# Kernel optimization log

Measured on AMD Instinct MI355X. Metric: run time of the kernel, lower is better.

The kernel has to match this reference:

```python
import jax, jax.numpy as jnp
import numpy as np

N_HEADS = 4
D_HEAD = 32  # out_features // n_heads = 128 // 4
NEG_SLOPE = 0.2


def setup_inputs() -> dict:
    key = jax.random.key(0)
    k_x, k_adj, k_w, k_a = jax.random.split(key, 4)
    B, N, F_in, F_out = 4, 2048, 128, 128
    x = jax.random.normal(k_x, (B, N, F_in), dtype=jnp.float32)
    adj = jax.random.randint(k_adj, (B, N, N), 0, 2, dtype=jnp.int32)
    # Linear weight stored as [in, out] (torch stores [out, in]; math identical: x @ W)
    w_scale = np.sqrt(2.0 / (F_in + F_out))  # xavier-ish
    W = jax.random.normal(k_w, (F_in, F_out), dtype=jnp.float32) * w_scale
    a = jax.random.normal(k_a, (N_HEADS, 2 * D_HEAD), dtype=jnp.float32) * np.sqrt(2.0 / (2 * D_HEAD))
    return {"x": x, "adj": adj, "W": W, "a": a}


def reference(x, adj, W, a):
    B, N, _ = x.shape
    # project and split heads: [B, H, N, D]
    h = jnp.einsum('bnf,fo->bno', x, W).reshape(B, N, N_HEADS, D_HEAD).transpose(0, 2, 1, 3)
    # additive attention logits
    e_src = jnp.einsum('bhnd,hd->bhn', h, a[:, :D_HEAD])  # [B,H,N]
    e_dst = jnp.einsum('bhnd,hd->bhn', h, a[:, D_HEAD:])  # [B,H,N]
    e = e_src[:, :, :, None] + e_dst[:, :, None, :]       # [B,H,N,N]
    e = jnp.where(e > 0, e, NEG_SLOPE * e)                # leaky_relu(0.2)
    mask = (adj[:, None, :, :] == 0)                      # [B,1,N,N] -> broadcast over heads
    e = jnp.where(mask, -jnp.inf, e)
    alpha = jax.nn.softmax(e, axis=-1)                    # dropout omitted (eval mode)
    out = jnp.einsum('bhnm,bhmd->bhnd', alpha, h)         # weighted aggregation
    out = out.transpose(0, 2, 1, 3).reshape(B, N, N_HEADS * D_HEAD)
    return jax.nn.elu(out)
```

## Files before the change

kernel.cpp:

```cpp
#include <hip/hip_runtime.h>
#include <hip/hip_bf16.h>

#define BB 4
#define NN 2048
#define FIN 128
#define NH 4
#define DH 32
#define NS 0.2f

typedef unsigned int u32;
typedef unsigned short u16;
typedef unsigned long long u64;
typedef __attribute__((ext_vector_type(8))) short short8;
typedef __attribute__((ext_vector_type(4))) float f32x4;

#define OFF_ES 0
#define OFF_ED 32768
#define OFF_P  65536
#define OFF_Q  98304
#define OFF_M  131072
#define OFF_HT 131088
#define OFF_BITS 655376

__device__ __forceinline__ u16 f2bf_rne(float f) {
  unsigned u = __float_as_uint(f);
  return (u16)((u + 0x7fffu + ((u >> 16) & 1u)) >> 16);
}

__global__ __launch_bounds__(256) void k_pack(const int* __restrict__ adj,
                                              u32* __restrict__ bits) {
  const int row = (blockIdx.x << 2) | (threadIdx.x >> 6);
  const int lane = threadIdx.x & 63;
  const int* src = adj + (size_t)row * NN;
  u32* dst = bits + (size_t)row * 64;
#pragma unroll 8
  for (int it = 0; it < 32; ++it) {
    const int v = src[it * 64 + lane];
    const u64 m = __ballot(v != 0);
    if (lane == 0) *(u64*)(dst + it * 2) = m;
  }
}

__global__ __launch_bounds__(256) void k_proj(
    const float* __restrict__ x, const float* __restrict__ W,
    const float* __restrict__ a, u16* __restrict__ hT,
    float* __restrict__ e_src, float* __restrict__ e_dst) {
  __shared__ float Ws[FIN * 128];
  const int tid = threadIdx.x;
  const int f = tid & 127, g = tid >> 7;
  const float4* Wg4 = (const float4*)W;
  float4* Ws4 = (float4*)Ws;
#pragma unroll
  for (int t = 0; t < 16; ++t) Ws4[t * 256 + tid] = Wg4[t * 256 + tid];
  __syncthreads();

  const int rb = blockIdx.x * 16 + g * 8;
  const int head = f >> 5, d = f & 31;
  const int b = rb >> 11, n0 = rb & (NN - 1);
  const int bh = b * NH + head;
  const float a_s = a[head * (2 * DH) + d];
  const float a_d = a[head * (2 * DH) + DH + d];

  float acc[8];
#pragma unroll
  for (int r = 0; r < 8; ++r) acc[r] = 0.f;

  const float* xb = x + (size_t)rb * FIN;
  for (int k = 0; k < FIN; ++k) {
    const float wv = Ws[k * 128 + f];
#pragma unroll
    for (int r = 0; r < 8; ++r) acc[r] = fmaf(wv, xb[r * FIN + k], acc[r]);
  }

  u16 hs[8];
#pragma unroll
  for (int r = 0; r < 8; ++r) hs[r] = f2bf_rne(acc[r]);
  u16* dst = hT + ((size_t)bh * DH + d) * NN + n0;
  *(int4*)dst = *(int4*)&hs[0];

#pragma unroll
  for (int r = 0; r < 8; ++r) {
    float s1 = acc[r] * a_s;
    float s2 = acc[r] * a_d;
#pragma unroll
    for (int off = 16; off >= 1; off >>= 1) {
      s1 += __shfl_xor(s1, off);
      s2 += __shfl_xor(s2, off);
    }
    if (d == 0) {
      e_src[(size_t)bh * NN + n0 + r] = s1;
      e_dst[(size_t)bh * NN + n0 + r] = s2;
    }
  }
}

__global__ __launch_bounds__(64) void k_prep(
    const float* __restrict__ e_dst, float* __restrict__ P,
    float* __restrict__ Q, float* __restrict__ M) {
  const int bh = blockIdx.x >> 3, seg = blockIdx.x & 7;
  const int lane = threadIdx.x;
  const float* ed = e_dst + (size_t)bh * NN;
  float m = -1e30f;
#pragma unroll
  for (int t = 0; t < 32; ++t) m = fmaxf(m, ed[t * 64 + lane]);
#pragma unroll
  for (int off = 32; off >= 1; off >>= 1) m = fmaxf(m, __shfl_xor(m, off));
  if (seg == 0 && lane == 0) M[bh] = m;
#pragma unroll
  for (int t = 0; t < 4; ++t) {
    const int j = seg * 256 + t * 64 + lane;
    const float e = ed[j];
    P[(size_t)bh * NN + j] = __expf(e);
    Q[(size_t)bh * NN + j] = __expf(NS * e);
  }
}

__global__ __launch_bounds__(256) void k_attn(
    const u16* __restrict__ hT, const float* __restrict__ e_src,
    const float* __restrict__ Pv, const float* __restrict__ Qv,
    const float* __restrict__ Mv, const u32* __restrict__ bits,
    float* __restrict__ out) {
  __shared__ float part[4][32][33];
  __shared__ float sp[4][2][16];

  const int bid = blockIdx.x;
  const int bh = bid >> 6;
  const int it = bid & 63;
  const int b = bh >> 2, head = bh & 3;

  const int w = threadIdx.x >> 6;
  const int lane = threadIdx.x & 63;
  const int lg = lane >> 4, lm = lane & 15;

  const int i0 = it * 32 + lm;
  const int i1 = i0 + 16;
  const float m = Mv[bh];
  const float es0 = e_src[(size_t)bh * NN + i0];
  const float es1 = e_src[(size_t)bh * NN + i1];
  const float mr0 = es0 + m, mr1 = es1 + m;
  const float mi0 = fmaxf(mr0, NS * mr0), mi1 = fmaxf(mr1, NS * mr1);
  const float A0 = __expf(es0 - mi0), B0 = __expf(NS * es0 - mi0);
  const float A1 = __expf(es1 - mi1), B1 = __expf(NS * es1 - mi1);
  const float T0 = __expf(-es0), T1 = __expf(-es1);

  const float* Pb = Pv + (size_t)bh * NN;
  const float* Qb = Qv + (size_t)bh * NN;
  const u16* hb0 = hT + ((size_t)bh * DH + lm) * NN;
  const u16* hb1 = hT + ((size_t)bh * DH + 16 + lm) * NN;
  const u32* br0 = bits + ((size_t)b * NN + i0) * 64 + w * 16;
  const u32* br1 = bits + ((size_t)b * NN + i1) * 64 + w * 16;
  const int shamt = lg * 8;

  f32x4 acc00 = {0,0,0,0}, acc01 = {0,0,0,0};
  f32x4 acc10 = {0,0,0,0}, acc11 = {0,0,0,0};
  float S0 = 0.f, S1 = 0.f;

  const int jbase = w * 512 + lg * 8;
  for (int jo = 0; jo < 4; ++jo) {
    const int4 bq0 = *(const int4*)(br0 + jo * 4);
    const int4 bq1 = *(const int4*)(br1 + jo * 4);
    const int wa0[4] = {bq0.x, bq0.y, bq0.z, bq0.w};
    const int wa1[4] = {bq1.x, bq1.y, bq1.z, bq1.w};
#pragma unroll
    for (int ju = 0; ju < 4; ++ju) {
      const int jj = jbase + jo * 128 + ju * 32;
      const float4 p0 = *(const float4*)(Pb + jj);
      const float4 p1 = *(const float4*)(Pb + jj + 4);
      const float4 q0 = *(const float4*)(Qb + jj);
      const float4 q1 = *(const float4*)(Qb + jj + 4);
      const short8 hv0 = *(const short8*)(hb0 + jj);
      const short8 hv1 = *(const short8*)(hb1 + jj);
      const u32 wsh0 = ((u32)wa0[ju]) >> shamt;
      const u32 wsh1 = ((u32)wa1[ju]) >> shamt;
      const float pp[8] = {p0.x, p0.y, p0.z, p0.w, p1.x, p1.y, p1.z, p1.w};
      const float qq[8] = {q0.x, q0.y, q0.z, q0.w, q1.x, q1.y, q1.z, q1.w};
      short8 af0, af1;
#pragma unroll
      for (int e = 0; e < 8; ++e) {
        const int m0 = (int)(wsh0 << (31 - e)) >> 31;
        const int m1 = (int)(wsh1 << (31 - e)) >> 31;
        const bool c0 = pp[e] > T0;
        float w0 = (c0 ? A0 : B0) * (c0 ? pp[e] : qq[e]);
        w0 = __int_as_float(__float_as_int(w0) & m0);
        S0 += w0;
        af0[e] = (short)__builtin_bit_cast(unsigned short, __float2bfloat16(w0));
        const bool c1 = pp[e] > T1;
        float w1 = (c1 ? A1 : B1) * (c1 ? pp[e] : qq[e]);
        w1 = __int_as_float(__float_as_int(w1) & m1);
        S1 += w1;
        af1[e] = (short)__builtin_bit_cast(unsigned short, __float2bfloat16(w1));
      }
      acc00 = __builtin_amdgcn_mfma_f32_16x16x32_bf16(af0, hv0, acc00, 0, 0, 0);
      acc01 = __builtin_amdgcn_mfma_f32_16x16x32_bf16(af0, hv1, acc01, 0, 0, 0);
      acc10 = __builtin_amdgcn_mfma_f32_16x16x32_bf16(af1, hv0, acc10, 0, 0, 0);
      acc11 = __builtin_amdgcn_mfma_f32_16x16x32_bf16(af1, hv1, acc11, 0, 0, 0);
    }
  }

  S0 += __shfl_xor(S0, 16); S0 += __shfl_xor(S0, 32);
  S1 += __shfl_xor(S1, 16); S1 += __shfl_xor(S1, 32);

#pragma unroll
  for (int r = 0; r < 4; ++r) {
    const int rl = lg * 4 + r;
    part[w][rl][lm] = acc00[r];
    part[w][rl][16 + lm] = acc01[r];
    part[w][16 + rl][lm] = acc10[r];
    part[w][16 + rl][16 + lm] = acc11[r];
  }
  if (lg == 0) { sp[w][0][lm] = S0; sp[w][1][lm] = S1; }
  __syncthreads();

  const int tid = threadIdx.x;
#pragma unroll
  for (int t = 0; t < 4; ++t) {
    const int idx = t * 256 + tid;
    const int row = idx >> 5, d = idx & 31;
    const float v = part[0][row][d] + part[1][row][d] +
                    part[2][row][d] + part[3][row][d];
    const float s = sp[0][row >> 4][row & 15] + sp[1][row >> 4][row & 15] +
                    sp[2][row >> 4][row & 15] + sp[3][row >> 4][row & 15];
    const float o = v / s;
    const int n = it * 32 + row;
    out[((size_t)b * NN + n) * 128 + head * 32 + d] =
        o > 0.f ? o : (__expf(o) - 1.f);
  }
}

extern "C" void kernel_launch(void* const* d_in, const int* in_sizes, int n_in,
                              void* d_out, int out_size, void* d_ws, size_t ws_size,
                              hipStream_t stream) {
  const float* x = (const float*)d_in[0];
  const int* adj = (const int*)d_in[1];
  const float* W = (const float*)d_in[2];
  const float* a = (const float*)d_in[3];
  float* out = (float*)d_out;
  float* ws = (float*)d_ws;

  float* e_src = ws + OFF_ES;
  float* e_dst = ws + OFF_ED;
  float* Pv = ws + OFF_P;
  float* Qv = ws + OFF_Q;
  float* Mv = ws + OFF_M;
  u16* hT = (u16*)(ws + OFF_HT);
  u32* bits = (u32*)(ws + OFF_BITS);

  k_pack<<<(BB * NN) / 4, 256, 0, stream>>>(adj, bits);
  k_proj<<<(BB * NN) / 16, 256, 0, stream>>>(x, W, a, hT, e_src, e_dst);
  k_prep<<<BB * NH * 8, 64, 0, stream>>>(e_dst, Pv, Qv, Mv);
  k_attn<<<BB * NH * 64, 256, 0, stream>>>(hT, e_src, Pv, Qv, Mv, bits, out);
}
```

Measured before the change: 69.05 us.

## Merge pack and projection kernels; simplify attention weight computation with fmax

Fuses the adjacency bit-packing and projection kernels into a single launch, interleaving one projection block with four packing blocks, so one launch is dropped and the two workloads overlap. In the attention loop, the branchy leaky-relu select becomes fmax(A*P, B*Q), which removes the per-row threshold exp. The loop is also flattened to 16 chunks with per-chunk bitmask loads, and the MFMA issue is wrapped in s_setprio. Every packing block still reserves the 64KB LDS array, which may limit occupancy for those blocks.

```diff
diff --git a/kernel.cpp b/kernel.cpp
--- a/kernel.cpp
+++ b/kernel.cpp
@@ -27,26 +27,31 @@
   return (u16)((u + 0x7fffu + ((u >> 16) & 1u)) >> 16);
 }
 
-__global__ __launch_bounds__(256) void k_pack(const int* __restrict__ adj,
-                                              u32* __restrict__ bits) {
-  const int row = (blockIdx.x << 2) | (threadIdx.x >> 6);
-  const int lane = threadIdx.x & 63;
-  const int* src = adj + (size_t)row * NN;
-  u32* dst = bits + (size_t)row * 64;
-#pragma unroll 8
-  for (int it = 0; it < 32; ++it) {
-    const int v = src[it * 64 + lane];
-    const u64 m = __ballot(v != 0);
-    if (lane == 0) *(u64*)(dst + it * 2) = m;
-  }
-}
-
-__global__ __launch_bounds__(256) void k_proj(
+__global__ __launch_bounds__(256) void k_pp(
+    const int* __restrict__ adj, u32* __restrict__ bits,
     const float* __restrict__ x, const float* __restrict__ W,
     const float* __restrict__ a, u16* __restrict__ hT,
     float* __restrict__ e_src, float* __restrict__ e_dst) {
   __shared__ float Ws[FIN * 128];
+  const int bid = blockIdx.x;
   const int tid = threadIdx.x;
+
+  if (bid % 5 != 0) {
+    const int pid = bid - bid / 5 - 1;
+    const int row = (pid << 2) | (tid >> 6);
+    const int lane = tid & 63;
+    const int* src = adj + (size_t)row * NN;
+    u32* dst = bits + (size_t)row * 64;
+#pragma unroll 8
+    for (int it = 0; it < 32; ++it) {
+      const int v = src[it * 64 + lane];
+      const u64 m = __ballot(v != 0);
+      if (lane == 0) *(u64*)(dst + it * 2) = m;
+    }
+    return;
+  }
+
+  const int pid = bid / 5;
   const int f = tid & 127, g = tid >> 7;
   const float4* Wg4 = (const float4*)W;
   float4* Ws4 = (float4*)Ws;
@@ -54,7 +59,7 @@
   for (int t = 0; t < 16; ++t) Ws4[t * 256 + tid] = Wg4[t * 256 + tid];
   __syncthreads();
 
-  const int rb = blockIdx.x * 16 + g * 8;
+  const int rb = pid * 16 + g * 8;
   const int head = f >> 5, d = f & 31;
   const int b = rb >> 11, n0 = rb & (NN - 1);
   const int bh = b * NH + head;
@@ -141,7 +146,6 @@
   const float mi0 = fmaxf(mr0, NS * mr0), mi1 = fmaxf(mr1, NS * mr1);
   const float A0 = __expf(es0 - mi0), B0 = __expf(NS * es0 - mi0);
   const float A1 = __expf(es1 - mi1), B1 = __expf(NS * es1 - mi1);
-  const float T0 = __expf(-es0), T1 = __expf(-es1);
 
   const float* Pb = Pv + (size_t)bh * NN;
   const float* Qb = Qv + (size_t)bh * NN;
@@ -156,45 +160,39 @@
   float S0 = 0.f, S1 = 0.f;
 
   const int jbase = w * 512 + lg * 8;
-  for (int jo = 0; jo < 4; ++jo) {
-    const int4 bq0 = *(const int4*)(br0 + jo * 4);
-    const int4 bq1 = *(const int4*)(br1 + jo * 4);
-    const int wa0[4] = {bq0.x, bq0.y, bq0.z, bq0.w};
-    const int wa1[4] = {bq1.x, bq1.y, bq1.z, bq1.w};
-#pragma unroll
-    for (int ju = 0; ju < 4; ++ju) {
-      const int jj = jbase + jo * 128 + ju * 32;
-      const float4 p0 = *(const float4*)(Pb + jj);
-      const float4 p1 = *(const float4*)(Pb + jj + 4);
-      const float4 q0 = *(const float4*)(Qb + jj);
-      const float4 q1 = *(const float4*)(Qb + jj + 4);
-      const short8 hv0 = *(const short8*)(hb0 + jj);
-      const short8 hv1 = *(const short8*)(hb1 + jj);
-      const u32 wsh0 = ((u32)wa0[ju]) >> shamt;
-      const u32 wsh1 = ((u32)wa1[ju]) >> shamt;
-      const float pp[8] = {p0.x, p0.y, p0.z, p0.w, p1.x, p1.y, p1.z, p1.w};
-      const float qq[8] = {q0.x, q0.y, q0.z, q0.w, q1.x, q1.y, q1.z, q1.w};
-      short8 af0, af1;
-#pragma unroll
-      for (int e = 0; e < 8; ++e) {
-        const int m0 = (int)(wsh0 << (31 - e)) >> 31;
-        const int m1 = (int)(wsh1 << (31 - e)) >> 31;
-        const bool c0 = pp[e] > T0;
-        float w0 = (c0 ? A0 : B0) * (c0 ? pp[e] : qq[e]);
-        w0 = __int_as_float(__float_as_int(w0) & m0);
-        S0 += w0;
-        af0[e] = (short)__builtin_bit_cast(unsigned short, __float2bfloat16(w0));
-        const bool c1 = pp[e] > T1;
-        float w1 = (c1 ? A1 : B1) * (c1 ? pp[e] : qq[e]);
-        w1 = __int_as_float(__float_as_int(w1) & m1);
-        S1 += w1;
-        af1[e] = (short)__builtin_bit_cast(unsigned short, __float2bfloat16(w1));
-      }
-      acc00 = __builtin_amdgcn_mfma_f32_16x16x32_bf16(af0, hv0, acc00, 0, 0, 0);
-      acc01 = __builtin_amdgcn_mfma_f32_16x16x32_bf16(af0, hv1, acc01, 0, 0, 0);
-      acc10 = __builtin_amdgcn_mfma_f32_16x16x32_bf16(af1, hv0, acc10, 0, 0, 0);
-      acc11 = __builtin_amdgcn_mfma_f32_16x16x32_bf16(af1, hv1, acc11, 0, 0, 0);
-    }
+#pragma unroll 2
+  for (int ch = 0; ch < 16; ++ch) {
+    const int jj = jbase + ch * 32;
+    const u32 wsh0 = br0[ch] >> shamt;
+    const u32 wsh1 = br1[ch] >> shamt;
+    const float4 p0 = *(const float4*)(Pb + jj);
+    const float4 p1 = *(const float4*)(Pb + jj + 4);
+    const float4 q0 = *(const float4*)(Qb + jj);
+    const float4 q1 = *(const float4*)(Qb + jj + 4);
+    const short8 hv0 = *(const short8*)(hb0 + jj);
+    const short8 hv1 = *(const short8*)(hb1 + jj);
+    const float pp[8] = {p0.x, p0.y, p0.z, p0.w, p1.x, p1.y, p1.z, p1.w};
+    const float qq[8] = {q0.x, q0.y, q0.z, q0.w, q1.x, q1.y, q1.z, q1.w};
+    short8 af0, af1;
+#pragma unroll
+    for (int e = 0; e < 8; ++e) {
+      const int m0 = (int)(wsh0 << (31 - e)) >> 31;
+      const int m1 = (int)(wsh1 << (31 - e)) >> 31;
+      float w0 = fmaxf(A0 * pp[e], B0 * qq[e]);
+      w0 = __int_as_float(__float_as_int(w0) & m0);
+      S0 += w0;
+      af0[e] = (short)__builtin_bit_cast(unsigned short, __float2bfloat16(w0));
+      float w1 = fmaxf(A1 * pp[e], B1 * qq[e]);
+      w1 = __int_as_float(__float_as_int(w1) & m1);
+      S1 += w1;
+      af1[e] = (short)__builtin_bit_cast(unsigned short, __float2bfloat16(w1));
+    }
+    __builtin_amdgcn_s_setprio(1);
+    acc00 = __builtin_amdgcn_mfma_f32_16x16x32_bf16(af0, hv0, acc00, 0, 0, 0);
+    acc01 = __builtin_amdgcn_mfma_f32_16x16x32_bf16(af0, hv1, acc01, 0, 0, 0);
+    acc10 = __builtin_amdgcn_mfma_f32_16x16x32_bf16(af1, hv0, acc10, 0, 0, 0);
+    acc11 = __builtin_amdgcn_mfma_f32_16x16x32_bf16(af1, hv1, acc11, 0, 0, 0);
+    __builtin_amdgcn_s_setprio(0);
   }
 
   S0 += __shfl_xor(S0, 16); S0 += __shfl_xor(S0, 32);
@@ -245,8 +243,7 @@
   u16* hT = (u16*)(ws + OFF_HT);
   u32* bits = (u32*)(ws + OFF_BITS);
 
-  k_pack<<<(BB * NN) / 4, 256, 0, stream>>>(adj, bits);
-  k_proj<<<(BB * NN) / 16, 256, 0, stream>>>(x, W, a, hT, e_src, e_dst);
+  k_pp<<<2560, 256, 0, stream>>>(adj, bits, x, W, a, hT, e_src, e_dst);
   k_prep<<<BB * NH * 8, 64, 0, stream>>>(e_dst, Pv, Qv, Mv);
   k_attn<<<BB * NH * 64, 256, 0, stream>>>(hT, e_src, Pv, Qv, Mv, bits, out);
 }
```

After: 106.6 us. 1.54x slower.

## Halve rows per attention block, use fmax for leaky-relu weights, raise MFMA priority

Applied to the files above, without the earlier changes.

Each attention block now handles 16 query rows instead of 32, which doubles the grid to 2048 blocks and halves per-thread register and accumulator state. The compare-and-select form of the leaky-relu exponent weight is replaced by fmaxf(A*P, B*Q), which relies on exp being monotonic and drops the T threshold exp. s_setprio brackets the MFMA calls so they are favoured when waves compete. In exchange, each block reloads the P, Q and hT data for only half as many rows, so global/L2 traffic per output row doubles.

```diff
diff --git a/kernel.cpp b/kernel.cpp
--- a/kernel.cpp
+++ b/kernel.cpp
@@ -120,47 +120,39 @@
     const float* __restrict__ Pv, const float* __restrict__ Qv,
     const float* __restrict__ Mv, const u32* __restrict__ bits,
     float* __restrict__ out) {
-  __shared__ float part[4][32][33];
-  __shared__ float sp[4][2][16];
+  __shared__ float part[4][16][33];
+  __shared__ float sp[4][16];
 
   const int bid = blockIdx.x;
-  const int bh = bid >> 6;
-  const int it = bid & 63;
+  const int bh = bid >> 7;
+  const int it = bid & 127;
   const int b = bh >> 2, head = bh & 3;
 
   const int w = threadIdx.x >> 6;
   const int lane = threadIdx.x & 63;
   const int lg = lane >> 4, lm = lane & 15;
 
-  const int i0 = it * 32 + lm;
-  const int i1 = i0 + 16;
+  const int i0 = it * 16 + lm;
   const float m = Mv[bh];
   const float es0 = e_src[(size_t)bh * NN + i0];
-  const float es1 = e_src[(size_t)bh * NN + i1];
-  const float mr0 = es0 + m, mr1 = es1 + m;
-  const float mi0 = fmaxf(mr0, NS * mr0), mi1 = fmaxf(mr1, NS * mr1);
+  const float mr0 = es0 + m;
+  const float mi0 = fmaxf(mr0, NS * mr0);
   const float A0 = __expf(es0 - mi0), B0 = __expf(NS * es0 - mi0);
-  const float A1 = __expf(es1 - mi1), B1 = __expf(NS * es1 - mi1);
-  const float T0 = __expf(-es0), T1 = __expf(-es1);
 
   const float* Pb = Pv + (size_t)bh * NN;
   const float* Qb = Qv + (size_t)bh * NN;
   const u16* hb0 = hT + ((size_t)bh * DH + lm) * NN;
   const u16* hb1 = hT + ((size_t)bh * DH + 16 + lm) * NN;
   const u32* br0 = bits + ((size_t)b * NN + i0) * 64 + w * 16;
-  const u32* br1 = bits + ((size_t)b * NN + i1) * 64 + w * 16;
   const int shamt = lg * 8;
 
   f32x4 acc00 = {0,0,0,0}, acc01 = {0,0,0,0};
-  f32x4 acc10 = {0,0,0,0}, acc11 = {0,0,0,0};
-  float S0 = 0.f, S1 = 0.f;
+  float S0 = 0.f;
 
   const int jbase = w * 512 + lg * 8;
   for (int jo = 0; jo < 4; ++jo) {
     const int4 bq0 = *(const int4*)(br0 + jo * 4);
-    const int4 bq1 = *(const int4*)(br1 + jo * 4);
     const int wa0[4] = {bq0.x, bq0.y, bq0.z, bq0.w};
-    const int wa1[4] = {bq1.x, bq1.y, bq1.z, bq1.w};
 #pragma unroll
     for (int ju = 0; ju < 4; ++ju) {
       const int jj = jbase + jo * 128 + ju * 32;
@@ -171,57 +163,46 @@
       const short8 hv0 = *(const short8*)(hb0 + jj);
       const short8 hv1 = *(const short8*)(hb1 + jj);
       const u32 wsh0 = ((u32)wa0[ju]) >> shamt;
-      const u32 wsh1 = ((u32)wa1[ju]) >> shamt;
       const float pp[8] = {p0.x, p0.y, p0.z, p0.w, p1.x, p1.y, p1.z, p1.w};
       const float qq[8] = {q0.x, q0.y, q0.z, q0.w, q1.x, q1.y, q1.z, q1.w};
-      short8 af0, af1;
+      short8 af0;
 #pragma unroll
       for (int e = 0; e < 8; ++e) {
         const int m0 = (int)(wsh0 << (31 - e)) >> 31;
-        const int m1 = (int)(wsh1 << (31 - e)) >> 31;
-        const bool c0 = pp[e] > T0;
-        float w0 = (c0 ? A0 : B0) * (c0 ? pp[e] : qq[e]);
+        float w0 = fmaxf(A0 * pp[e], B0 * qq[e]);
         w0 = __int_as_float(__float_as_int(w0) & m0);
         S0 += w0;
         af0[e] = (short)__builtin_bit_cast(unsigned short, __float2bfloat16(w0));
-        const bool c1 = pp[e] > T1;
-        float w1 = (c1 ? A1 : B1) * (c1 ? pp[e] : qq[e]);
-        w1 = __int_as_float(__float_as_int(w1) & m1);
-        S1 += w1;
-        af1[e] = (short)__builtin_bit_cast(unsigned short, __float2bfloat16(w1));
       }
+      __builtin_amdgcn_s_setprio(1);
       acc00 = __builtin_amdgcn_mfma_f32_16x16x32_bf16(af0, hv0, acc00, 0, 0, 0);
       acc01 = __builtin_amdgcn_mfma_f32_16x16x32_bf16(af0, hv1, acc01, 0, 0, 0);
-      acc10 = __builtin_amdgcn_mfma_f32_16x16x32_bf16(af1, hv0, acc10, 0, 0, 0);
-      acc11 = __builtin_amdgcn_mfma_f32_16x16x32_bf16(af1, hv1, acc11, 0, 0, 0);
+      __builtin_amdgcn_s_setprio(0);
     }
   }
 
-  S0 += __shfl_xor(S0, 16); S0 += __shfl_xor(S0, 32);
-  S1 += __shfl_xor(S1, 16); S1 += __shfl_xor(S1, 32);
+  S0 += __shfl_xor(S0, 16);
+  S0 += __shfl_xor(S0, 32);
 
 #pragma unroll
   for (int r = 0; r < 4; ++r) {
     const int rl = lg * 4 + r;
     part[w][rl][lm] = acc00[r];
     part[w][rl][16 + lm] = acc01[r];
-    part[w][16 + rl][lm] = acc10[r];
-    part[w][16 + rl][16 + lm] = acc11[r];
-  }
-  if (lg == 0) { sp[w][0][lm] = S0; sp[w][1][lm] = S1; }
+  }
+  if (lg == 0) sp[w][lm] = S0;
   __syncthreads();
 
   const int tid = threadIdx.x;
 #pragma unroll
-  for (int t = 0; t < 4; ++t) {
+  for (int t = 0; t < 2; ++t) {
     const int idx = t * 256 + tid;
     const int row = idx >> 5, d = idx & 31;
     const float v = part[0][row][d] + part[1][row][d] +
                     part[2][row][d] + part[3][row][d];
-    const float s = sp[0][row >> 4][row & 15] + sp[1][row >> 4][row & 15] +
-                    sp[2][row >> 4][row & 15] + sp[3][row >> 4][row & 15];
+    const float s = sp[0][row] + sp[1][row] + sp[2][row] + sp[3][row];
     const float o = v / s;
-    const int n = it * 32 + row;
+    const int n = it * 16 + row;
     out[((size_t)b * NN + n) * 128 + head * 32 + d] =
         o > 0.f ? o : (__expf(o) - 1.f);
   }
@@ -248,5 +229,5 @@
   k_pack<<<(BB * NN) / 4, 256, 0, stream>>>(adj, bits);
   k_proj<<<(BB * NN) / 16, 256, 0, stream>>>(x, W, a, hT, e_src, e_dst);
   k_prep<<<BB * NH * 8, 64, 0, stream>>>(e_dst, Pv, Qv, Mv);
-  k_attn<<<BB * NH * 64, 256, 0, stream>>>(hT, e_src, Pv, Qv, Mv, bits, out);
-}
+  k_attn<<<BB * NH * 128, 256, 0, stream>>>(hT, e_src, Pv, Qv, Mv, bits, out);
+}
```

New measurement: 88.69 us. 1.28x slower.

## Pack P/Q exp tables as bf16 pairs and software-pipeline attention loads

Applied to the files above, without the earlier changes.

Stores exp(e_dst) and exp(0.2*e_dst) as two bf16 halves of a single u32, halving that table's traffic in the attention kernel. The leaky-relu branch select becomes a max of the two scaled products. All adjacency bit words are preloaded, and the next chunk's PQ and h loads are double-buffered so they overlap the current chunk's compute. MFMA issue is also wrapped in s_setprio. Rounding the exp tables to bf16 adds precision loss to the attention weights, and the extra prefetch buffers raise register pressure.

```diff
diff --git a/kernel.cpp b/kernel.cpp
--- a/kernel.cpp
+++ b/kernel.cpp
@@ -13,11 +13,11 @@
 typedef unsigned long long u64;
 typedef __attribute__((ext_vector_type(8))) short short8;
 typedef __attribute__((ext_vector_type(4))) float f32x4;
+typedef __attribute__((ext_vector_type(4))) unsigned int u32x4;
 
 #define OFF_ES 0
 #define OFF_ED 32768
-#define OFF_P  65536
-#define OFF_Q  98304
+#define OFF_PQ 65536
 #define OFF_M  131072
 #define OFF_HT 131088
 #define OFF_BITS 655376
@@ -25,6 +25,14 @@
 __device__ __forceinline__ u16 f2bf_rne(float f) {
   unsigned u = __float_as_uint(f);
   return (u16)((u + 0x7fffu + ((u >> 16) & 1u)) >> 16);
+}
+
+__device__ __forceinline__ int sign_bit(u32 w, int e) {
+#if __has_builtin(__builtin_amdgcn_sbfe)
+  return __builtin_amdgcn_sbfe((int)w, e, 1);
+#else
+  return ((int)(w << (31 - e))) >> 31;
+#endif
 }
 
 __global__ __launch_bounds__(256) void k_pack(const int* __restrict__ adj,
@@ -95,8 +103,8 @@
 }
 
 __global__ __launch_bounds__(64) void k_prep(
-    const float* __restrict__ e_dst, float* __restrict__ P,
-    float* __restrict__ Q, float* __restrict__ M) {
+    const float* __restrict__ e_dst, u32* __restrict__ PQ,
+    float* __restrict__ M) {
   const int bh = blockIdx.x >> 3, seg = blockIdx.x & 7;
   const int lane = threadIdx.x;
   const float* ed = e_dst + (size_t)bh * NN;
@@ -110,16 +118,16 @@
   for (int t = 0; t < 4; ++t) {
     const int j = seg * 256 + t * 64 + lane;
     const float e = ed[j];
-    P[(size_t)bh * NN + j] = __expf(e);
-    Q[(size_t)bh * NN + j] = __expf(NS * e);
+    const u32 pb = f2bf_rne(__expf(e));
+    const u32 qb = f2bf_rne(__expf(NS * e));
+    PQ[(size_t)bh * NN + j] = (qb << 16) | pb;
   }
 }
 
 __global__ __launch_bounds__(256) void k_attn(
     const u16* __restrict__ hT, const float* __restrict__ e_src,
-    const float* __restrict__ Pv, const float* __restrict__ Qv,
-    const float* __restrict__ Mv, const u32* __restrict__ bits,
-    float* __restrict__ out) {
+    const u32* __restrict__ PQv, const float* __restrict__ Mv,
+    const u32* __restrict__ bits, float* __restrict__ out) {
   __shared__ float part[4][32][33];
   __shared__ float sp[4][2][16];
 
@@ -141,60 +149,70 @@
   const float mi0 = fmaxf(mr0, NS * mr0), mi1 = fmaxf(mr1, NS * mr1);
   const float A0 = __expf(es0 - mi0), B0 = __expf(NS * es0 - mi0);
   const float A1 = __expf(es1 - mi1), B1 = __expf(NS * es1 - mi1);
-  const float T0 = __expf(-es0), T1 = __expf(-es1);
-
-  const float* Pb = Pv + (size_t)bh * NN;
-  const float* Qb = Qv + (size_t)bh * NN;
+
+  const u32* PQb = PQv + (size_t)bh * NN;
   const u16* hb0 = hT + ((size_t)bh * DH + lm) * NN;
   const u16* hb1 = hT + ((size_t)bh * DH + 16 + lm) * NN;
   const u32* br0 = bits + ((size_t)b * NN + i0) * 64 + w * 16;
   const u32* br1 = bits + ((size_t)b * NN + i1) * 64 + w * 16;
   const int shamt = lg * 8;
 
+  u32 wd0[16], wd1[16];
+#pragma unroll
+  for (int jo = 0; jo < 4; ++jo) {
+    const u32x4 v0 = *(const u32x4*)(br0 + jo * 4);
+    const u32x4 v1 = *(const u32x4*)(br1 + jo * 4);
+#pragma unroll
+    for (int k = 0; k < 4; ++k) { wd0[jo * 4 + k] = v0[k]; wd1[jo * 4 + k] = v1[k]; }
+  }
+
   f32x4 acc00 = {0,0,0,0}, acc01 = {0,0,0,0};
   f32x4 acc10 = {0,0,0,0}, acc11 = {0,0,0,0};
   float S0 = 0.f, S1 = 0.f;
 
   const int jbase = w * 512 + lg * 8;
-  for (int jo = 0; jo < 4; ++jo) {
-    const int4 bq0 = *(const int4*)(br0 + jo * 4);
-    const int4 bq1 = *(const int4*)(br1 + jo * 4);
-    const int wa0[4] = {bq0.x, bq0.y, bq0.z, bq0.w};
-    const int wa1[4] = {bq1.x, bq1.y, bq1.z, bq1.w};
-#pragma unroll
-    for (int ju = 0; ju < 4; ++ju) {
-      const int jj = jbase + jo * 128 + ju * 32;
-      const float4 p0 = *(const float4*)(Pb + jj);
-      const float4 p1 = *(const float4*)(Pb + jj + 4);
-      const float4 q0 = *(const float4*)(Qb + jj);
-      const float4 q1 = *(const float4*)(Qb + jj + 4);
-      const short8 hv0 = *(const short8*)(hb0 + jj);
-      const short8 hv1 = *(const short8*)(hb1 + jj);
-      const u32 wsh0 = ((u32)wa0[ju]) >> shamt;
-      const u32 wsh1 = ((u32)wa1[ju]) >> shamt;
-      const float pp[8] = {p0.x, p0.y, p0.z, p0.w, p1.x, p1.y, p1.z, p1.w};
-      const float qq[8] = {q0.x, q0.y, q0.z, q0.w, q1.x, q1.y, q1.z, q1.w};
-      short8 af0, af1;
-#pragma unroll
-      for (int e = 0; e < 8; ++e) {
-        const int m0 = (int)(wsh0 << (31 - e)) >> 31;
-        const int m1 = (int)(wsh1 << (31 - e)) >> 31;
-        const bool c0 = pp[e] > T0;
-        float w0 = (c0 ? A0 : B0) * (c0 ? pp[e] : qq[e]);
-        w0 = __int_as_float(__float_as_int(w0) & m0);
-        S0 += w0;
-        af0[e] = (short)__builtin_bit_cast(unsigned short, __float2bfloat16(w0));
-        const bool c1 = pp[e] > T1;
-        float w1 = (c1 ? A1 : B1) * (c1 ? pp[e] : qq[e]);
-        w1 = __int_as_float(__float_as_int(w1) & m1);
-        S1 += w1;
-        af1[e] = (short)__builtin_bit_cast(unsigned short, __float2bfloat16(w1));
-      }
-      acc00 = __builtin_amdgcn_mfma_f32_16x16x32_bf16(af0, hv0, acc00, 0, 0, 0);
-      acc01 = __builtin_amdgcn_mfma_f32_16x16x32_bf16(af0, hv1, acc01, 0, 0, 0);
-      acc10 = __builtin_amdgcn_mfma_f32_16x16x32_bf16(af1, hv0, acc10, 0, 0, 0);
-      acc11 = __builtin_amdgcn_mfma_f32_16x16x32_bf16(af1, hv1, acc11, 0, 0, 0);
-    }
+
+  u32x4 pqa_c = *(const u32x4*)(PQb + jbase);
+  u32x4 pqb_c = *(const u32x4*)(PQb + jbase + 4);
+  short8 h0_c = *(const short8*)(hb0 + jbase);
+  short8 h1_c = *(const short8*)(hb1 + jbase);
+
+#pragma unroll
+  for (int c = 0; c < 16; ++c) {
+    u32x4 pqa_n, pqb_n; short8 h0_n, h1_n;
+    if (c < 15) {
+      const int jn = jbase + (c + 1) * 32;
+      pqa_n = *(const u32x4*)(PQb + jn);
+      pqb_n = *(const u32x4*)(PQb + jn + 4);
+      h0_n = *(const short8*)(hb0 + jn);
+      h1_n = *(const short8*)(hb1 + jn);
+    }
+    const u32 wsh0 = wd0[c] >> shamt;
+    const u32 wsh1 = wd1[c] >> shamt;
+    short8 af0, af1;
+#pragma unroll
+    for (int e = 0; e < 8; ++e) {
+      const u32 pq = (e < 4) ? pqa_c[e] : pqb_c[e - 4];
+      const float Pf = __uint_as_float(pq << 16);
+      const float Qf = __uint_as_float(pq & 0xffff0000u);
+      const int m0 = sign_bit(wsh0, e);
+      const int m1 = sign_bit(wsh1, e);
+      float w0 = fmaxf(A0 * Pf, B0 * Qf);
+      w0 = __int_as_float(__float_as_int(w0) & m0);
+      S0 += w0;
+      af0[e] = (short)__builtin_bit_cast(unsigned short, __float2bfloat16(w0));
+      float w1 = fmaxf(A1 * Pf, B1 * Qf);
+      w1 = __int_as_float(__float_as_int(w1) & m1);
+      S1 += w1;
+      af1[e] = (short)__builtin_bit_cast(unsigned short, __float2bfloat16(w1));
+    }
+    __builtin_amdgcn_s_setprio(1);
+    acc00 = __builtin_amdgcn_mfma_f32_16x16x32_bf16(af0, h0_c, acc00, 0, 0, 0);
+    acc01 = __builtin_amdgcn_mfma_f32_16x16x32_bf16(af0, h1_c, acc01, 0, 0, 0);
+    acc10 = __builtin_amdgcn_mfma_f32_16x16x32_bf16(af1, h0_c, acc10, 0, 0, 0);
+    acc11 = __builtin_amdgcn_mfma_f32_16x16x32_bf16(af1, h1_c, acc11, 0, 0, 0);
+    __builtin_amdgcn_s_setprio(0);
+    if (c < 15) { pqa_c = pqa_n; pqb_c = pqb_n; h0_c = h0_n; h1_c = h1_n; }
   }
 
   S0 += __shfl_xor(S0, 16); S0 += __shfl_xor(S0, 32);
@@ -239,14 +257,13 @@
 
   float* e_src = ws + OFF_ES;
   float* e_dst = ws + OFF_ED;
-  float* Pv = ws + OFF_P;
-  float* Qv = ws + OFF_Q;
+  u32* PQv = (u32*)(ws + OFF_PQ);
   float* Mv = ws + OFF_M;
   u16* hT = (u16*)(ws + OFF_HT);
   u32* bits = (u32*)(ws + OFF_BITS);
 
   k_pack<<<(BB * NN) / 4, 256, 0, stream>>>(adj, bits);
   k_proj<<<(BB * NN) / 16, 256, 0, stream>>>(x, W, a, hT, e_src, e_dst);
-  k_prep<<<BB * NH * 8, 64, 0, stream>>>(e_dst, Pv, Qv, Mv);
-  k_attn<<<BB * NH * 64, 256, 0, stream>>>(hT, e_src, Pv, Qv, Mv, bits, out);
-}
+  k_prep<<<BB * NH * 8, 64, 0, stream>>>(e_dst, PQv, Mv);
+  k_attn<<<BB * NH * 64, 256, 0, stream>>>(hT, e_src, PQv, Mv, bits, out);
+}
```

After: 64.79 us. -6.2%, faster.
